# Kernel tuning notes

Hardware: AMD Instinct MI355X
Metric: run time of the kernel (lower is better)

The kernel has to match this reference:

```python
import jax, jax.numpy as jnp
import numpy as np

HEAD_DIM = 32
KERNEL = 3
DILATION = 2
SCALE = HEAD_DIM ** -0.5


def _unfold(x, kernel, dilation):
    # x: [B, C, H, W] -> patches [B, C, kernel*kernel, H, W]
    # matches nn.Unfold(kernel, dilation, padding=dilation*(kernel-1)//2, stride=1)
    B, C, H, W = x.shape
    pad = dilation * (kernel - 1) // 2
    xp = jnp.pad(x, ((0, 0), (0, 0), (pad, pad), (pad, pad)))
    patches = jnp.stack(
        [xp[:, :, i * dilation:i * dilation + H, j * dilation:j * dilation + W]
         for i in range(kernel) for j in range(kernel)],
        axis=2,
    )
    return patches  # [B, C, k*k, H, W]


def setup_inputs() -> dict:
    key = jax.random.key(0)
    kq, kk, kv = jax.random.split(key, 3)
    shape = (8, 192, 56, 56)
    return {
        "q": jax.random.normal(kq, shape, dtype=jnp.float32),
        "k": jax.random.normal(kk, shape, dtype=jnp.float32),
        "v": jax.random.normal(kv, shape, dtype=jnp.float32),
    }


def reference(q, k, v):
    B, d, H, W = q.shape
    h = d // HEAD_DIM
    kk2 = KERNEL * KERNEL
    HW = H * W

    # q: [B, h, hd, HW]
    qh = q.reshape(B, h, HEAD_DIM, HW)
    # unfolded k/v: [B, h, hd, k*k, HW]
    kp = _unfold(k, KERNEL, DILATION).reshape(B, h, HEAD_DIM, kk2, HW)
    vp = _unfold(v, KERNEL, DILATION).reshape(B, h, HEAD_DIM, kk2, HW)

    attn = jnp.einsum('bhdn,bhdkn->bhnk', qh, kp) * SCALE
    attn = jax.nn.softmax(attn, axis=-1)
    # dropout p=0 (eval): no-op

    # [B, h, HW, hd]
    out = jnp.einsum('bhnk,bhdkn->bhnd', attn, vp)
    # transpose(1,2).reshape(B,H,W,d): channel order = head-major
    out = out.transpose(0, 2, 1, 3).reshape(B, H, W, d)
    return out
```

## Files before the change

kernel.cpp:

```cpp
#include <hip/hip_runtime.h>

#define NH 6
#define HEAD_DIM 32
#define CCH 192
#define HH 56
#define WW 56
#define HWSZ (HH * WW)
#define KPOS 9
#define SCALE 0.17677669529663687f
#define XPAD 61
#define ROWSZ (HEAD_DIM * XPAD)
#define NROWS 4
#define PAIRS 14

__global__ __launch_bounds__(512, 4) void dilate_attn_pair(
    const float* __restrict__ q,
    const float* __restrict__ k,
    const float* __restrict__ v,
    float* __restrict__ out)
{
    __shared__ float ks[NROWS * ROWSZ];
    __shared__ float vs[NROWS * ROWSZ];

    const int bh       = blockIdx.x % 48;
    const int pair_lin = blockIdx.x / 48;
    const int parity   = pair_lin / PAIRS;
    const int p        = pair_lin % PAIRS;
    const int y0       = 4 * p + parity;
    const int t        = threadIdx.x;

    const size_t plane = (size_t)bh * HEAD_DIM * HWSZ;
#pragma unroll
    for (int i = 0; i < 14; i++) {
        const int e   = t + 512 * i;
        const int r   = e / 1792;
        const int rem = e - r * 1792;
        const int d   = rem / WW;
        const int x   = rem - d * WW;
        const int sy  = y0 - 2 + 2 * r;
        const bool okr = (sy >= 0) & (sy < HH);
        const size_t g = plane + (size_t)d * HWSZ + (okr ? sy : 0) * WW + x;
        const float kvv = okr ? k[g] : 0.0f;
        const float vvv = okr ? v[g] : 0.0f;
        const int a = r * ROWSZ + d * XPAD + x + 2;
        ks[a] = kvv;
        vs[a] = vvv;
    }
    {
        const int r  = t >> 7;
        const int rs = t & 127;
        const int d  = rs >> 2;
        const int xc = rs & 3;
        const int xp = (xc < 2) ? xc : (56 + xc);
        ks[r * ROWSZ + d * XPAD + xp] = 0.0f;
        vs[r * ROWSZ + d * XPAD + xp] = 0.0f;
    }
    __syncthreads();

    const int w2 = t >> 8;
    const int tt = t & 255;
    const int px = tt >> 2;
    const int c  = tt & 3;
    if (px >= WW) return;

    const int y = y0 + 2 * w2;

    float qreg[8];
    {
        const float* qb = q + plane + (size_t)(8 * c) * HWSZ + y * WW + px;
#pragma unroll
        for (int j = 0; j < 8; j++) qreg[j] = qb[j * HWSZ];
    }

    float lg[KPOS];
#pragma unroll
    for (int rr = 0; rr < 3; rr++) {
        const float* kr = ks + (w2 + rr) * ROWSZ + (8 * c) * XPAD + px;
        float a0 = 0.f, a1 = 0.f, a2 = 0.f;
#pragma unroll
        for (int j = 0; j < 8; j++) {
            const float* pp = kr + j * XPAD;
            const float qj = qreg[j];
            a0 = fmaf(qj, pp[0], a0);
            a1 = fmaf(qj, pp[2], a1);
            a2 = fmaf(qj, pp[4], a2);
        }
        lg[3 * rr + 0] = a0;
        lg[3 * rr + 1] = a1;
        lg[3 * rr + 2] = a2;
    }

#pragma unroll
    for (int kk = 0; kk < KPOS; kk++) {
        float s = lg[kk];
        s += __shfl_xor(s, 1);
        s += __shfl_xor(s, 2);
        lg[kk] = s * SCALE;
    }

    float m = lg[0];
#pragma unroll
    for (int kk = 1; kk < KPOS; kk++) m = fmaxf(m, lg[kk]);
    float ssum = 0.f;
    float w[KPOS];
#pragma unroll
    for (int kk = 0; kk < KPOS; kk++) {
        w[kk] = __expf(lg[kk] - m);
        ssum += w[kk];
    }
    const float inv = 1.f / ssum;
#pragma unroll
    for (int kk = 0; kk < KPOS; kk++) w[kk] *= inv;

    float acc[8];
#pragma unroll
    for (int j = 0; j < 8; j++) acc[j] = 0.f;
#pragma unroll
    for (int rr = 0; rr < 3; rr++) {
        const float* vr = vs + (w2 + rr) * ROWSZ + (8 * c) * XPAD + px;
        const float w0 = w[3 * rr + 0];
        const float w1 = w[3 * rr + 1];
        const float w2f = w[3 * rr + 2];
#pragma unroll
        for (int j = 0; j < 8; j++) {
            const float* pp = vr + j * XPAD;
            float a = acc[j];
            a = fmaf(w0,  pp[0], a);
            a = fmaf(w1,  pp[2], a);
            a = fmaf(w2f, pp[4], a);
            acc[j] = a;
        }
    }

    const int h = bh % NH;
    const int b = bh / NH;
    float* ob = out + ((size_t)((b * HH + y) * WW + px)) * CCH
                    + h * HEAD_DIM + 8 * c;
    reinterpret_cast<float4*>(ob)[0] = make_float4(acc[0], acc[1], acc[2], acc[3]);
    reinterpret_cast<float4*>(ob)[1] = make_float4(acc[4], acc[5], acc[6], acc[7]);
}

extern "C" void kernel_launch(void* const* d_in, const int* in_sizes, int n_in,
                              void* d_out, int out_size, void* d_ws, size_t ws_size,
                              hipStream_t stream) {
    const float* q = (const float*)d_in[0];
    const float* k = (const float*)d_in[1];
    const float* v = (const float*)d_in[2];
    float* out = (float*)d_out;

    const int blocks = 48 * 2 * PAIRS;
    dilate_attn_pair<<<blocks, 512, 0, stream>>>(q, k, v, out);
}
```

Baseline: 116.5 us.

## Split width into halves, transpose LDS to channel-contiguous with float4 reads

```diff
diff --git a/kernel.cpp b/kernel.cpp
--- a/kernel.cpp
+++ b/kernel.cpp
@@ -8,86 +8,87 @@
 #define HWSZ (HH * WW)
 #define KPOS 9
 #define SCALE 0.17677669529663687f
-#define XPAD 61
-#define ROWSZ (HEAD_DIM * XPAD)
+#define DSTR 36
+#define XCOLS 32
+#define ROWF (XCOLS * DSTR)
 #define NROWS 4
 #define PAIRS 14
+#define XOUT 28
 
-__global__ __launch_bounds__(512, 4) void dilate_attn_pair(
+__global__ __launch_bounds__(256, 4) void dilate_attn_v7(
     const float* __restrict__ q,
     const float* __restrict__ k,
     const float* __restrict__ v,
     float* __restrict__ out)
 {
-    __shared__ float ks[NROWS * ROWSZ];
-    __shared__ float vs[NROWS * ROWSZ];
+    __shared__ __align__(16) float ks[NROWS * ROWF];
+    __shared__ __align__(16) float vs[NROWS * ROWF];
 
-    const int bh       = blockIdx.x % 48;
-    const int pair_lin = blockIdx.x / 48;
-    const int parity   = pair_lin / PAIRS;
-    const int p        = pair_lin % PAIRS;
-    const int y0       = 4 * p + parity;
-    const int t        = threadIdx.x;
+    const int bh  = blockIdx.x % 48;
+    const int r1  = blockIdx.x / 48;
+    const int xh  = r1 & 1;
+    const int pl  = r1 >> 1;
+    const int parity = pl / PAIRS;
+    const int p      = pl % PAIRS;
+    const int y0  = 4 * p + parity;
+    const int x0  = xh * XOUT;
+    const int t   = threadIdx.x;
 
     const size_t plane = (size_t)bh * HEAD_DIM * HWSZ;
-#pragma unroll
-    for (int i = 0; i < 14; i++) {
-        const int e   = t + 512 * i;
-        const int r   = e / 1792;
-        const int rem = e - r * 1792;
-        const int d   = rem / WW;
-        const int x   = rem - d * WW;
-        const int sy  = y0 - 2 + 2 * r;
-        const bool okr = (sy >= 0) & (sy < HH);
-        const size_t g = plane + (size_t)d * HWSZ + (okr ? sy : 0) * WW + x;
-        const float kvv = okr ? k[g] : 0.0f;
-        const float vvv = okr ? v[g] : 0.0f;
-        const int a = r * ROWSZ + d * XPAD + x + 2;
-        ks[a] = kvv;
-        vs[a] = vvv;
-    }
-    {
-        const int r  = t >> 7;
-        const int rs = t & 127;
-        const int d  = rs >> 2;
-        const int xc = rs & 3;
-        const int xp = (xc < 2) ? xc : (56 + xc);
-        ks[r * ROWSZ + d * XPAD + xp] = 0.0f;
-        vs[r * ROWSZ + d * XPAD + xp] = 0.0f;
-    }
-    __syncthreads();
 
-    const int w2 = t >> 8;
-    const int tt = t & 255;
-    const int px = tt >> 2;
-    const int c  = tt & 3;
-    if (px >= WW) return;
-
-    const int y = y0 + 2 * w2;
+    const int w2  = t >> 7;
+    const int tt  = t & 127;
+    const int pxl = tt >> 2;
+    const int c   = tt & 3;
+    const int y   = y0 + 2 * w2;
+    const int gx  = x0 + pxl;
+    const bool active = pxl < XOUT;
 
     float qreg[8];
-    {
-        const float* qb = q + plane + (size_t)(8 * c) * HWSZ + y * WW + px;
+    if (active) {
+        const float* qb = q + plane + (size_t)(8 * c) * HWSZ + y * WW + gx;
 #pragma unroll
         for (int j = 0; j < 8; j++) qreg[j] = qb[j * HWSZ];
     }
 
+#pragma unroll
+    for (int i = 0; i < 16; i++) {
+        const int e = t + 256 * i;
+        const int x = e & 31;
+        const int d = (e >> 5) & 31;
+        const int r = e >> 10;
+        const int sy = y0 - 2 + 2 * r;
+        const int sx = x0 - 2 + x;
+        const bool ok = (sy >= 0) & (sy < HH) & (sx >= 0) & (sx < WW);
+        const size_t g = plane + (size_t)d * HWSZ + (ok ? (sy * WW + sx) : 0);
+        const float kvv = ok ? k[g] : 0.0f;
+        const float vvv = ok ? v[g] : 0.0f;
+        const int a = r * ROWF + x * DSTR + d;
+        ks[a] = kvv;
+        vs[a] = vvv;
+    }
+    __syncthreads();
+
+    if (!active) return;
+
     float lg[KPOS];
 #pragma unroll
     for (int rr = 0; rr < 3; rr++) {
-        const float* kr = ks + (w2 + rr) * ROWSZ + (8 * c) * XPAD + px;
-        float a0 = 0.f, a1 = 0.f, a2 = 0.f;
 #pragma unroll
-        for (int j = 0; j < 8; j++) {
-            const float* pp = kr + j * XPAD;
-            const float qj = qreg[j];
-            a0 = fmaf(qj, pp[0], a0);
-            a1 = fmaf(qj, pp[2], a1);
-            a2 = fmaf(qj, pp[4], a2);
+        for (int ix = 0; ix < 3; ix++) {
+            const float* kp = ks + (w2 + rr) * ROWF + (pxl + 2 * ix) * DSTR + 8 * c;
+            const float4 k0 = *reinterpret_cast<const float4*>(kp);
+            const float4 k1 = *reinterpret_cast<const float4*>(kp + 4);
+            float a = qreg[0] * k0.x;
+            a = fmaf(qreg[1], k0.y, a);
+            a = fmaf(qreg[2], k0.z, a);
+            a = fmaf(qreg[3], k0.w, a);
+            a = fmaf(qreg[4], k1.x, a);
+            a = fmaf(qreg[5], k1.y, a);
+            a = fmaf(qreg[6], k1.z, a);
+            a = fmaf(qreg[7], k1.w, a);
+            lg[3 * rr + ix] = a;
         }
-        lg[3 * rr + 0] = a0;
-        lg[3 * rr + 1] = a1;
-        lg[3 * rr + 2] = a2;
     }
 
 #pragma unroll
@@ -112,32 +113,33 @@
 #pragma unroll
     for (int kk = 0; kk < KPOS; kk++) w[kk] *= inv;
 
-    float acc[8];
-#pragma unroll
-    for (int j = 0; j < 8; j++) acc[j] = 0.f;
+    float a0 = 0.f, a1 = 0.f, a2 = 0.f, a3 = 0.f;
+    float a4 = 0.f, a5 = 0.f, a6 = 0.f, a7 = 0.f;
 #pragma unroll
     for (int rr = 0; rr < 3; rr++) {
-        const float* vr = vs + (w2 + rr) * ROWSZ + (8 * c) * XPAD + px;
-        const float w0 = w[3 * rr + 0];
-        const float w1 = w[3 * rr + 1];
-        const float w2f = w[3 * rr + 2];
 #pragma unroll
-        for (int j = 0; j < 8; j++) {
-            const float* pp = vr + j * XPAD;
-            float a = acc[j];
-            a = fmaf(w0,  pp[0], a);
-            a = fmaf(w1,  pp[2], a);
-            a = fmaf(w2f, pp[4], a);
-            acc[j] = a;
+        for (int ix = 0; ix < 3; ix++) {
+            const float* vp = vs + (w2 + rr) * ROWF + (pxl + 2 * ix) * DSTR + 8 * c;
+            const float4 v0 = *reinterpret_cast<const float4*>(vp);
+            const float4 v1 = *reinterpret_cast<const float4*>(vp + 4);
+            const float wk = w[3 * rr + ix];
+            a0 = fmaf(wk, v0.x, a0);
+            a1 = fmaf(wk, v0.y, a1);
+            a2 = fmaf(wk, v0.z, a2);
+            a3 = fmaf(wk, v0.w, a3);
+            a4 = fmaf(wk, v1.x, a4);
+            a5 = fmaf(wk, v1.y, a5);
+            a6 = fmaf(wk, v1.z, a6);
+            a7 = fmaf(wk, v1.w, a7);
         }
     }
 
     const int h = bh % NH;
     const int b = bh / NH;
-    float* ob = out + ((size_t)((b * HH + y) * WW + px)) * CCH
+    float* ob = out + ((size_t)((b * HH + y) * WW + gx)) * CCH
                     + h * HEAD_DIM + 8 * c;
-    reinterpret_cast<float4*>(ob)[0] = make_float4(acc[0], acc[1], acc[2], acc[3]);
-    reinterpret_cast<float4*>(ob)[1] = make_float4(acc[4], acc[5], acc[6], acc[7]);
+    reinterpret_cast<float4*>(ob)[0] = make_float4(a0, a1, a2, a3);
+    reinterpret_cast<float4*>(ob)[1] = make_float4(a4, a5, a6, a7);
 }
 
 extern "C" void kernel_launch(void* const* d_in, const int* in_sizes, int n_in,
@@ -148,6 +150,6 @@
     const float* v = (const float*)d_in[2];
     float* out = (float*)d_out;
 
-    const int blocks = 48 * 2 * PAIRS;
-    dilate_attn_pair<<<blocks, 512, 0, stream>>>(q, k, v, out);
+    const int blocks = 48 * 2 * PAIRS * 2;
+    dilate_attn_v7<<<blocks, 256, 0, stream>>>(q, k, v, out);
 }
```

Result: no change. 118.0 us (+1.3%).
